# Kernel optimization log

Measured on AMD Instinct MI355X. Metric: run time of the kernel, lower is better.

Reference implementation:

```python
import jax, jax.numpy as jnp
import numpy as np

N_NODES = 100000
N_EDGES = 1600000
IN_DIM = 128
HID_DIM = 128
OUT_DIM = 16
N_GRAPHS = 128


def setup_inputs() -> dict:
    key = jax.random.key(0)
    ks = jax.random.split(key, 8)
    x = jax.random.normal(ks[0], (N_NODES, IN_DIM), dtype=jnp.float32)
    edge_index = jax.random.randint(ks[1], (2, N_EDGES), 0, N_NODES, dtype=jnp.int64)
    batch = jnp.sort(jax.random.randint(ks[2], (N_NODES,), 0, N_GRAPHS, dtype=jnp.int64))
    # GCNConv params (glorot-ish scale) and Linear params
    w1 = jax.random.normal(ks[3], (IN_DIM, HID_DIM), dtype=jnp.float32) / np.sqrt(IN_DIM)
    b1 = jnp.zeros((HID_DIM,), dtype=jnp.float32)
    w2 = jax.random.normal(ks[4], (HID_DIM, HID_DIM), dtype=jnp.float32) / np.sqrt(HID_DIM)
    b2 = jnp.zeros((HID_DIM,), dtype=jnp.float32)
    wc = jax.random.normal(ks[5], (HID_DIM, OUT_DIM), dtype=jnp.float32) / np.sqrt(HID_DIM)
    bc = jnp.zeros((OUT_DIM,), dtype=jnp.float32)
    return {"x": x, "edge_index": edge_index, "batch": batch,
            "w1": w1, "b1": b1, "w2": w2, "b2": b2, "wc": wc, "bc": bc}


def _gcn_layer(h, src, dst, w, b, n_nodes):
    # h: [N, Fin]; src/dst: [E+N] (self-loops already appended)
    h = h @ w  # [N, Fout]
    ones = jnp.ones_like(dst, dtype=h.dtype)
    deg = jax.ops.segment_sum(ones, dst, num_segments=n_nodes)  # [N]
    dinv = jnp.where(deg > 0, jax.lax.rsqrt(deg), 0.0)
    norm = dinv[src] * dinv[dst]  # [E+N]
    msg = h[src] * norm[:, None]  # gather + scale, [E+N, Fout]
    out = jax.ops.segment_sum(msg, dst, num_segments=n_nodes)  # scatter-add
    return out + b


def reference(x, edge_index, batch, w1, b1, w2, b2, wc, bc):
    n = x.shape[0]
    loop = jnp.arange(n, dtype=edge_index.dtype)
    src = jnp.concatenate([edge_index[0], loop])  # add self-loops (PyG default)
    dst = jnp.concatenate([edge_index[1], loop])

    h = jax.nn.relu(_gcn_layer(x, src, dst, w1, b1, n))
    h = jax.nn.relu(_gcn_layer(h, src, dst, w2, b2, n))

    # global mean pool over graphs
    sums = jax.ops.segment_sum(h, batch, num_segments=N_GRAPHS)  # [G, H]
    cnt = jax.ops.segment_sum(jnp.ones((n,), h.dtype), batch, num_segments=N_GRAPHS)
    pooled = sums / jnp.maximum(cnt, 1.0)[:, None]

    return pooled @ wc + bc  # [G, OUT_DIM]
```

## Files before the change

kernel.cpp:

```cpp
#include <hip/hip_runtime.h>
#include <stdint.h>

#define NN 100000
#define NE 1600000
#define FDIM 128
#define NGRAPH 128
#define ODIM 16
#define NBKT 391
#define CAP 4608
#define PCAP 8704
#define SCHUNK 2048
#define NSCAT ((NE + SCHUNK - 1) / SCHUNK)
#define NSTARTB ((NN + 255) / 256)

typedef __attribute__((ext_vector_type(8))) short short8;
typedef __attribute__((ext_vector_type(8))) unsigned short ushort8;
typedef __attribute__((ext_vector_type(4))) float f32x4;
typedef __attribute__((ext_vector_type(2))) float f32x2;

__device__ __forceinline__ float blo(unsigned int p) { return __uint_as_float(p << 16); }
__device__ __forceinline__ float bhi(unsigned int p) { return __uint_as_float(p & 0xffff0000u); }
__device__ __forceinline__ unsigned short f2b(float f) {
    unsigned int u = __float_as_uint(f);
    unsigned int r = (u + 0x7fffu + ((u >> 16) & 1u)) >> 16;
    return (unsigned short)r;
}
__device__ __forceinline__ unsigned int packbf(float lo, float hi) {
    return (unsigned int)f2b(lo) | ((unsigned int)f2b(hi) << 16);
}

__device__ __forceinline__ int detect_w(const int* __restrict__ ei) {
    int lane = threadIdx.x & 63;
    int v = ei[2 * lane + 1];
    return (__ballot(v != 0) == 0ULL) ? 1 : 0;
}
__device__ __forceinline__ int ld_idx(const int* __restrict__ p, long long i, int w) {
    return w ? p[2 * i] : p[i];
}

__global__ void __launch_bounds__(256) k_prep(
    const float* __restrict__ w1, const float* __restrict__ w2,
    unsigned short* __restrict__ wt1, unsigned short* __restrict__ wt2,
    const int* __restrict__ ei, const int* __restrict__ batch,
    int* __restrict__ gstart, int* __restrict__ bcursor,
    unsigned short* __restrict__ xws)
{
    int b = blockIdx.x, t = threadIdx.x;
    if (b < 128) {
        int idx = b * 256 + t;
        int which = idx >> 14, r = idx & 16383;
        int k = r >> 7, j = r & 127;
        const float* w = which ? w2 : w1;
        unsigned short* wt = which ? wt2 : wt1;
        wt[j * 128 + k] = f2b(w[k * 128 + j]);
    } else if (b < 128 + NSTARTB) {
        int w = detect_w(ei);
        int i = (b - 128) * 256 + t;
        if (i < NN) {
            int bb = ld_idx(batch, i, w);
            int prev = (i == 0) ? -1 : ld_idx(batch, i - 1, w);
            for (int g = prev + 1; g <= bb; ++g) gstart[g] = i;
            if (i == NN - 1)
                for (int g = bb + 1; g <= NGRAPH; ++g) gstart[g] = NN;
        }
    } else {
        int i = (b - 128 - NSTARTB) * 256 + t;
        if (i < NBKT) bcursor[i] = i * CAP;
        if (b == 128 + NSTARTB && t < FDIM) xws[(size_t)NN * FDIM + t] = 0;
    }
}

__global__ void __launch_bounds__(512) k_scat(const int* __restrict__ ei,
                                              int* __restrict__ bcursor,
                                              unsigned int* __restrict__ rec) {
    __shared__ int hist[NBKT];
    __shared__ int gbase[NBKT];
    __shared__ int lcur[NBKT];
    int t = threadIdx.x;
    int w = detect_w(ei);
    for (int i = t; i < NBKT; i += 512) hist[i] = 0;
    __syncthreads();
    long long e0 = (long long)blockIdx.x * SCHUNK;
    unsigned int myrec[4];
    int mybkt[4];
    #pragma unroll
    for (int j = 0; j < 4; ++j) {
        long long e = e0 + j * 512 + t;
        if (e < NE) {
            int s = ld_idx(ei, e, w);
            int d = ld_idx(ei, NE + e, w);
            mybkt[j] = d >> 8;
            myrec[j] = (unsigned int)s | ((unsigned int)(d & 255) << 17);
            atomicAdd(&hist[mybkt[j]], 1);
        } else mybkt[j] = -1;
    }
    __syncthreads();
    for (int i = t; i < NBKT; i += 512) {
        int c = hist[i];
        gbase[i] = c ? atomicAdd(&bcursor[i], c) : 0;
        lcur[i] = 0;
    }
    __syncthreads();
    #pragma unroll
    for (int j = 0; j < 4; ++j) {
        int b = mybkt[j];
        if (b >= 0) {
            int r = atomicAdd(&lcur[b], 1);
            int p = gbase[b] + r;
            if (p < (b + 1) * CAP) rec[p] = myrec[j];
        }
    }
}

__global__ void __launch_bounds__(256) k_bucket(const unsigned int* __restrict__ rec,
                                                const int* __restrict__ bcursor,
                                                int* __restrict__ csr,
                                                int* __restrict__ offs,
                                                int* __restrict__ deg,
                                                float* __restrict__ dinv) {
    __shared__ unsigned int rbuf[CAP];
    __shared__ int srcout[PCAP];
    __shared__ int hist[256], scn[256], cur[256];
    int b = blockIdx.x, t = threadIdx.x;
    int rbase = b * CAP;
    int cnt = bcursor[b] - rbase;
    if (cnt > CAP) cnt = CAP;
    hist[t] = 0;
    __syncthreads();
    for (int j = t; j < cnt; j += 256) {
        unsigned int r = rec[rbase + j];
        rbuf[j] = r;
        atomicAdd(&hist[r >> 17], 1);
    }
    for (int j = t; j < PCAP; j += 256) srcout[j] = NN << 8;
    __syncthreads();
    int node = (b << 8) + t;
    int v = hist[t];
    int pv = (node < NN) ? ((v + 16) & ~15) : 0;
    scn[t] = pv;
    __syncthreads();
    for (int o = 1; o < 256; o <<= 1) {
        int tv = (t >= o) ? scn[t - o] : 0;
        __syncthreads();
        scn[t] += tv;
        __syncthreads();
    }
    int pexcl = scn[t] - pv;
    cur[t] = pexcl;
    int obase = b * PCAP;
    if (node < NN) {
        offs[node] = obase + pexcl;
        deg[node] = pv;
        dinv[node] = rsqrtf((float)(v + 1));
        srcout[pexcl + v] = node << 8;
    }
    __syncthreads();
    for (int j = t; j < cnt; j += 256) {
        unsigned int r = rbuf[j];
        int p = atomicAdd(&cur[r >> 17], 1);
        srcout[p] = (int)(r & 0x1FFFFu) << 8;
    }
    __syncthreads();
    int total = scn[255];
    for (int j = t; j < total; j += 256) csr[obase + j] = srcout[j];
}

#define LWS 136
template <bool BF16IN>
__global__ void __launch_bounds__(256) k_gemm(
    const void* __restrict__ Xv,
    const unsigned short* __restrict__ WT,
    const float* __restrict__ dinv,
    unsigned short* __restrict__ OUT)
{
    __shared__ unsigned short lw[128 * LWS];
    int tid = threadIdx.x;
    for (int it = 0; it < 8; ++it) {
        int vidx = it * 256 + tid;
        int j = vidx >> 4, kc = vidx & 15;
        ushort8 v = *(const ushort8*)(WT + j * 128 + kc * 8);
        *(ushort8*)(&lw[j * LWS + kc * 8]) = v;
    }
    __syncthreads();

    int wave = tid >> 6, lane = tid & 63;
    int quad = lane >> 4, n16 = lane & 15;
    int row0 = (blockIdx.x * 4 + wave) * 16;
    if (row0 >= NN) return;

    f32x4 acc[8];
    for (int ct = 0; ct < 8; ++ct) acc[ct] = (f32x4){0.f, 0.f, 0.f, 0.f};

    const int arow = row0 + n16;
    for (int kk = 0; kk < 4; ++kk) {
        short8 a;
        if (BF16IN) {
            a = *(const short8*)((const unsigned short*)Xv + (size_t)arow * 128 + kk * 32 + quad * 8);
        } else {
            const float* ap = (const float*)Xv + (size_t)arow * 128 + kk * 32 + quad * 8;
            float4 a01 = *(const float4*)(ap);
            float4 a23 = *(const float4*)(ap + 4);
            a[0] = (short)f2b(a01.x); a[1] = (short)f2b(a01.y);
            a[2] = (short)f2b(a01.z); a[3] = (short)f2b(a01.w);
            a[4] = (short)f2b(a23.x); a[5] = (short)f2b(a23.y);
            a[6] = (short)f2b(a23.z); a[7] = (short)f2b(a23.w);
        }
        for (int ct = 0; ct < 8; ++ct) {
            short8 b = *(const short8*)(&lw[(ct * 16 + n16) * LWS + kk * 32 + quad * 8]);
            acc[ct] = __builtin_amdgcn_mfma_f32_16x16x32_bf16(a, b, acc[ct], 0, 0, 0);
        }
    }
    for (int r = 0; r < 4; ++r) {
        int row = row0 + quad * 4 + r;
        float dv = dinv[row];
        for (int ct = 0; ct < 8; ++ct)
            OUT[(size_t)row * 128 + ct * 16 + n16] = f2b(acc[ct][r] * dv);
    }
}

__device__ __forceinline__ void acc8(f32x2* a2, uint4 q) {
    a2[0] += (f32x2){blo(q.x), bhi(q.x)};
    a2[1] += (f32x2){blo(q.y), bhi(q.y)};
    a2[2] += (f32x2){blo(q.z), bhi(q.z)};
    a2[3] += (f32x2){blo(q.w), bhi(q.w)};
}

__global__ void __launch_bounds__(256) k_agg(
    const unsigned short* __restrict__ XWS,
    const int* __restrict__ csr,
    const int* __restrict__ offs,
    const int* __restrict__ deg,
    const float* __restrict__ dinv,
    const float* __restrict__ bias,
    unsigned short* __restrict__ H)
{
    int wave = threadIdx.x >> 6, lane = threadIdx.x & 63;
    int v = blockIdx.x * 4 + wave;
    int g = lane >> 4, f = lane & 15;
    int beg = offs[v], pdeg = deg[v];
    const char* xb = (const char*)XWS;
    unsigned fo = (unsigned)(f * 16);
    const int* cp = csr + beg + 4 * g;

    f32x2 a2[4];
    a2[0] = (f32x2){0.f, 0.f}; a2[1] = (f32x2){0.f, 0.f};
    a2[2] = (f32x2){0.f, 0.f}; a2[3] = (f32x2){0.f, 0.f};

    for (int j = 0; j < pdeg; j += 16) {
        int4 c = *(const int4*)(cp + j);
        uint4 q0 = *(const uint4*)(xb + ((unsigned)c.x + fo));
        uint4 q1 = *(const uint4*)(xb + ((unsigned)c.y + fo));
        uint4 q2 = *(const uint4*)(xb + ((unsigned)c.z + fo));
        uint4 q3 = *(const uint4*)(xb + ((unsigned)c.w + fo));
        acc8(a2, q0);
        acc8(a2, q1);
        acc8(a2, q2);
        acc8(a2, q3);
    }
    #pragma unroll
    for (int i = 0; i < 4; ++i) {
        a2[i].x += __shfl_xor(a2[i].x, 16);
        a2[i].y += __shfl_xor(a2[i].y, 16);
        a2[i].x += __shfl_xor(a2[i].x, 32);
        a2[i].y += __shfl_xor(a2[i].y, 32);
    }
    if (g == 0) {
        float dv = dinv[v];
        float4 b0 = *(const float4*)(bias + f * 8);
        float4 b1 = *(const float4*)(bias + f * 8 + 4);
        uint4 o;
        o.x = packbf(fmaxf(fmaf(a2[0].x, dv, b0.x), 0.f), fmaxf(fmaf(a2[0].y, dv, b0.y), 0.f));
        o.y = packbf(fmaxf(fmaf(a2[1].x, dv, b0.z), 0.f), fmaxf(fmaf(a2[1].y, dv, b0.w), 0.f));
        o.z = packbf(fmaxf(fmaf(a2[2].x, dv, b1.x), 0.f), fmaxf(fmaf(a2[2].y, dv, b1.y), 0.f));
        o.w = packbf(fmaxf(fmaf(a2[3].x, dv, b1.z), 0.f), fmaxf(fmaf(a2[3].y, dv, b1.w), 0.f));
        *(uint4*)(H + (size_t)v * FDIM + f * 8) = o;
    }
}

__global__ void __launch_bounds__(256) k_poolcls(
    const unsigned short* __restrict__ H, const int* __restrict__ gstart,
    const float* __restrict__ wc, const float* __restrict__ bc,
    float* __restrict__ out)
{
    __shared__ float red[512];
    __shared__ float pl[FDIM];
    int g = blockIdx.x;
    int t = threadIdx.x;
    int pair = t & 63;
    int seg = t >> 6;
    int beg = gstart[g], end = gstart[g + 1];
    float a0 = 0.f, a1 = 0.f;
    for (int i = beg + seg; i < end; i += 4) {
        unsigned int q = *(const unsigned int*)(H + (size_t)i * FDIM + 2 * pair);
        a0 += blo(q); a1 += bhi(q);
    }
    red[t] = a0; red[256 + t] = a1;
    __syncthreads();
    if (seg == 0) {
        a0 = red[t] + red[t + 64] + red[t + 128] + red[t + 192];
        a1 = red[256 + t] + red[256 + t + 64] + red[256 + t + 128] + red[256 + t + 192];
        float inv = 1.f / fmaxf((float)(end - beg), 1.f);
        pl[2 * pair] = a0 * inv;
        pl[2 * pair + 1] = a1 * inv;
    }
    __syncthreads();
    int o = t & 15, fs = t >> 4;
    float acc = 0.f;
    #pragma unroll
    for (int k = 0; k < 8; ++k)
        acc += pl[fs * 8 + k] * wc[(fs * 8 + k) * ODIM + o];
    red[t] = acc;
    __syncthreads();
    if (t < 16) {
        float s = bc[t];
        #pragma unroll
        for (int k = 0; k < 16; ++k) s += red[k * 16 + t];
        out[g * ODIM + t] = s;
    }
}

extern "C" void kernel_launch(void* const* d_in, const int* in_sizes, int n_in,
                              void* d_out, int out_size, void* d_ws, size_t ws_size,
                              hipStream_t stream) {
    const float* x   = (const float*)d_in[0];
    const int* ei    = (const int*)d_in[1];
    const int* batch = (const int*)d_in[2];
    const float* w1  = (const float*)d_in[3];
    const float* b1  = (const float*)d_in[4];
    const float* w2  = (const float*)d_in[5];
    const float* b2  = (const float*)d_in[6];
    const float* wc  = (const float*)d_in[7];
    const float* bc  = (const float*)d_in[8];
    float* out = (float*)d_out;

    char* ws = (char*)d_ws;
    size_t off = 0;
    auto alloc = [&](size_t bytes) -> void* {
        off = (off + 255) & ~(size_t)255;
        void* p = ws + off;
        off += bytes;
        return p;
    };
    int*   bcursor = (int*)alloc(NBKT * 4);
    int*   offs    = (int*)alloc(NN * 4);
    int*   deg     = (int*)alloc(NN * 4);
    float* dinv    = (float*)alloc(NN * 4);
    int*   gstart  = (int*)alloc((NGRAPH + 1) * 4);
    unsigned int* rec = (unsigned int*)alloc((size_t)NBKT * CAP * 4);
    int*   csr     = (int*)alloc((size_t)NBKT * PCAP * 4 + 256);
    unsigned short* wt1 = (unsigned short*)alloc(128 * 128 * 2);
    unsigned short* wt2 = (unsigned short*)alloc(128 * 128 * 2);
    unsigned short* xws = (unsigned short*)alloc((size_t)(NN + 1) * FDIM * 2);
    unsigned short* h   = (unsigned short*)alloc((size_t)NN * FDIM * 2);

    k_prep<<<128 + NSTARTB + 2, 256, 0, stream>>>(w1, w2, wt1, wt2, ei, batch, gstart, bcursor, xws);
    k_scat<<<NSCAT, 512, 0, stream>>>(ei, bcursor, rec);
    k_bucket<<<NBKT, 256, 0, stream>>>(rec, bcursor, csr, offs, deg, dinv);

    k_gemm<false><<<(NN / 16 + 3) / 4, 256, 0, stream>>>(x, wt1, dinv, xws);
    k_agg<<<NN / 4, 256, 0, stream>>>(xws, csr, offs, deg, dinv, b1, h);
    k_gemm<true><<<(NN / 16 + 3) / 4, 256, 0, stream>>>(h, wt2, dinv, xws);
    k_agg<<<NN / 4, 256, 0, stream>>>(xws, csr, offs, deg, dinv, b2, h);
    k_poolcls<<<NGRAPH, 256, 0, stream>>>(h, gstart, wc, bc, out);
}
```

Before: 342.3 us.

## Unroll aggregation gathers, pack offsets/degree, widen scatter and pool blocks

The aggregation loop is unrolled to issue eight row gathers per iteration, and the CSR index reads use nontemporal loads. Offsets and padded degree are packed into one int2 so each node needs a single load. The scatter kernel handles twice as many edges per block, and the pooling kernel runs 512 threads. Manual bf16 rounding is replaced with the HIP packed float2-to-bf16 conversion. The changes aim to raise memory-level parallelism and cut instruction count, at the cost of extra register pressure and fewer scatter blocks.

```diff
diff --git a/kernel.cpp b/kernel.cpp
--- a/kernel.cpp
+++ b/kernel.cpp
@@ -1,4 +1,5 @@
 #include <hip/hip_runtime.h>
+#include <hip/hip_bf16.h>
 #include <stdint.h>
 
 #define NN 100000
@@ -9,7 +10,7 @@
 #define NBKT 391
 #define CAP 4608
 #define PCAP 8704
-#define SCHUNK 2048
+#define SCHUNK 4096
 #define NSCAT ((NE + SCHUNK - 1) / SCHUNK)
 #define NSTARTB ((NN + 255) / 256)
 
@@ -17,6 +18,7 @@
 typedef __attribute__((ext_vector_type(8))) unsigned short ushort8;
 typedef __attribute__((ext_vector_type(4))) float f32x4;
 typedef __attribute__((ext_vector_type(2))) float f32x2;
+typedef __attribute__((ext_vector_type(4))) int i32x4;
 
 __device__ __forceinline__ float blo(unsigned int p) { return __uint_as_float(p << 16); }
 __device__ __forceinline__ float bhi(unsigned int p) { return __uint_as_float(p & 0xffff0000u); }
@@ -25,8 +27,9 @@
     unsigned int r = (u + 0x7fffu + ((u >> 16) & 1u)) >> 16;
     return (unsigned short)r;
 }
-__device__ __forceinline__ unsigned int packbf(float lo, float hi) {
-    return (unsigned int)f2b(lo) | ((unsigned int)f2b(hi) << 16);
+__device__ __forceinline__ unsigned int cvt2(float lo, float hi) {
+    __hip_bfloat162 b = __float22bfloat162_rn(float2{lo, hi});
+    return *reinterpret_cast<unsigned int*>(&b);
 }
 
 __device__ __forceinline__ int detect_w(const int* __restrict__ ei) {
@@ -81,10 +84,10 @@
     for (int i = t; i < NBKT; i += 512) hist[i] = 0;
     __syncthreads();
     long long e0 = (long long)blockIdx.x * SCHUNK;
-    unsigned int myrec[4];
-    int mybkt[4];
+    unsigned int myrec[8];
+    int mybkt[8];
     #pragma unroll
-    for (int j = 0; j < 4; ++j) {
+    for (int j = 0; j < 8; ++j) {
         long long e = e0 + j * 512 + t;
         if (e < NE) {
             int s = ld_idx(ei, e, w);
@@ -102,7 +105,7 @@
     }
     __syncthreads();
     #pragma unroll
-    for (int j = 0; j < 4; ++j) {
+    for (int j = 0; j < 8; ++j) {
         int b = mybkt[j];
         if (b >= 0) {
             int r = atomicAdd(&lcur[b], 1);
@@ -115,8 +118,7 @@
 __global__ void __launch_bounds__(256) k_bucket(const unsigned int* __restrict__ rec,
                                                 const int* __restrict__ bcursor,
                                                 int* __restrict__ csr,
-                                                int* __restrict__ offs,
-                                                int* __restrict__ deg,
+                                                int2* __restrict__ odeg,
                                                 float* __restrict__ dinv) {
     __shared__ unsigned int rbuf[CAP];
     __shared__ int srcout[PCAP];
@@ -128,7 +130,7 @@
     hist[t] = 0;
     __syncthreads();
     for (int j = t; j < cnt; j += 256) {
-        unsigned int r = rec[rbase + j];
+        unsigned int r = __builtin_nontemporal_load(&rec[rbase + j]);
         rbuf[j] = r;
         atomicAdd(&hist[r >> 17], 1);
     }
@@ -149,8 +151,7 @@
     cur[t] = pexcl;
     int obase = b * PCAP;
     if (node < NN) {
-        offs[node] = obase + pexcl;
-        deg[node] = pv;
+        odeg[node] = make_int2(obase + pexcl, pv);
         dinv[node] = rsqrtf((float)(v + 1));
         srcout[pexcl + v] = node << 8;
     }
@@ -200,10 +201,12 @@
             const float* ap = (const float*)Xv + (size_t)arow * 128 + kk * 32 + quad * 8;
             float4 a01 = *(const float4*)(ap);
             float4 a23 = *(const float4*)(ap + 4);
-            a[0] = (short)f2b(a01.x); a[1] = (short)f2b(a01.y);
-            a[2] = (short)f2b(a01.z); a[3] = (short)f2b(a01.w);
-            a[4] = (short)f2b(a23.x); a[5] = (short)f2b(a23.y);
-            a[6] = (short)f2b(a23.z); a[7] = (short)f2b(a23.w);
+            uint4 P;
+            P.x = cvt2(a01.x, a01.y);
+            P.y = cvt2(a01.z, a01.w);
+            P.z = cvt2(a23.x, a23.y);
+            P.w = cvt2(a23.z, a23.w);
+            a = *(short8*)&P;
         }
         for (int ct = 0; ct < 8; ++ct) {
             short8 b = *(const short8*)(&lw[(ct * 16 + n16) * LWS + kk * 32 + quad * 8]);
@@ -228,8 +231,7 @@
 __global__ void __launch_bounds__(256) k_agg(
     const unsigned short* __restrict__ XWS,
     const int* __restrict__ csr,
-    const int* __restrict__ offs,
-    const int* __restrict__ deg,
+    const int2* __restrict__ odeg,
     const float* __restrict__ dinv,
     const float* __restrict__ bias,
     unsigned short* __restrict__ H)
@@ -237,7 +239,8 @@
     int wave = threadIdx.x >> 6, lane = threadIdx.x & 63;
     int v = blockIdx.x * 4 + wave;
     int g = lane >> 4, f = lane & 15;
-    int beg = offs[v], pdeg = deg[v];
+    int2 od = odeg[v];
+    int beg = od.x, pdeg = od.y;
     const char* xb = (const char*)XWS;
     unsigned fo = (unsigned)(f * 16);
     const int* cp = csr + beg + 4 * g;
@@ -246,16 +249,29 @@
     a2[0] = (f32x2){0.f, 0.f}; a2[1] = (f32x2){0.f, 0.f};
     a2[2] = (f32x2){0.f, 0.f}; a2[3] = (f32x2){0.f, 0.f};
 
-    for (int j = 0; j < pdeg; j += 16) {
-        int4 c = *(const int4*)(cp + j);
-        uint4 q0 = *(const uint4*)(xb + ((unsigned)c.x + fo));
-        uint4 q1 = *(const uint4*)(xb + ((unsigned)c.y + fo));
-        uint4 q2 = *(const uint4*)(xb + ((unsigned)c.z + fo));
-        uint4 q3 = *(const uint4*)(xb + ((unsigned)c.w + fo));
-        acc8(a2, q0);
-        acc8(a2, q1);
-        acc8(a2, q2);
-        acc8(a2, q3);
+    int j = 0;
+    int pd2 = pdeg & ~31;
+    for (; j < pd2; j += 32) {
+        i32x4 ca = __builtin_nontemporal_load((const i32x4*)(cp + j));
+        i32x4 cb = __builtin_nontemporal_load((const i32x4*)(cp + j + 16));
+        uint4 q0 = *(const uint4*)(xb + ((unsigned)ca.x + fo));
+        uint4 q1 = *(const uint4*)(xb + ((unsigned)ca.y + fo));
+        uint4 q2 = *(const uint4*)(xb + ((unsigned)ca.z + fo));
+        uint4 q3 = *(const uint4*)(xb + ((unsigned)ca.w + fo));
+        uint4 q4 = *(const uint4*)(xb + ((unsigned)cb.x + fo));
+        uint4 q5 = *(const uint4*)(xb + ((unsigned)cb.y + fo));
+        uint4 q6 = *(const uint4*)(xb + ((unsigned)cb.z + fo));
+        uint4 q7 = *(const uint4*)(xb + ((unsigned)cb.w + fo));
+        acc8(a2, q0); acc8(a2, q1); acc8(a2, q2); acc8(a2, q3);
+        acc8(a2, q4); acc8(a2, q5); acc8(a2, q6); acc8(a2, q7);
+    }
+    if (j < pdeg) {
+        i32x4 ca = __builtin_nontemporal_load((const i32x4*)(cp + j));
+        uint4 q0 = *(const uint4*)(xb + ((unsigned)ca.x + fo));
+        uint4 q1 = *(const uint4*)(xb + ((unsigned)ca.y + fo));
+        uint4 q2 = *(const uint4*)(xb + ((unsigned)ca.z + fo));
+        uint4 q3 = *(const uint4*)(xb + ((unsigned)ca.w + fo));
+        acc8(a2, q0); acc8(a2, q1); acc8(a2, q2); acc8(a2, q3);
     }
     #pragma unroll
     for (int i = 0; i < 4; ++i) {
@@ -269,20 +285,20 @@
         float4 b0 = *(const float4*)(bias + f * 8);
         float4 b1 = *(const float4*)(bias + f * 8 + 4);
         uint4 o;
-        o.x = packbf(fmaxf(fmaf(a2[0].x, dv, b0.x), 0.f), fmaxf(fmaf(a2[0].y, dv, b0.y), 0.f));
-        o.y = packbf(fmaxf(fmaf(a2[1].x, dv, b0.z), 0.f), fmaxf(fmaf(a2[1].y, dv, b0.w), 0.f));
-        o.z = packbf(fmaxf(fmaf(a2[2].x, dv, b1.x), 0.f), fmaxf(fmaf(a2[2].y, dv, b1.y), 0.f));
-        o.w = packbf(fmaxf(fmaf(a2[3].x, dv, b1.z), 0.f), fmaxf(fmaf(a2[3].y, dv, b1.w), 0.f));
+        o.x = cvt2(fmaxf(fmaf(a2[0].x, dv, b0.x), 0.f), fmaxf(fmaf(a2[0].y, dv, b0.y), 0.f));
+        o.y = cvt2(fmaxf(fmaf(a2[1].x, dv, b0.z), 0.f), fmaxf(fmaf(a2[1].y, dv, b0.w), 0.f));
+        o.z = cvt2(fmaxf(fmaf(a2[2].x, dv, b1.x), 0.f), fmaxf(fmaf(a2[2].y, dv, b1.y), 0.f));
+        o.w = cvt2(fmaxf(fmaf(a2[3].x, dv, b1.z), 0.f), fmaxf(fmaf(a2[3].y, dv, b1.w), 0.f));
         *(uint4*)(H + (size_t)v * FDIM + f * 8) = o;
     }
 }
 
-__global__ void __launch_bounds__(256) k_poolcls(
+__global__ void __launch_bounds__(512) k_poolcls(
     const unsigned short* __restrict__ H, const int* __restrict__ gstart,
     const float* __restrict__ wc, const float* __restrict__ bc,
     float* __restrict__ out)
 {
-    __shared__ float red[512];
+    __shared__ float red[1024];
     __shared__ float pl[FDIM];
     int g = blockIdx.x;
     int t = threadIdx.x;
@@ -290,26 +306,32 @@
     int seg = t >> 6;
     int beg = gstart[g], end = gstart[g + 1];
     float a0 = 0.f, a1 = 0.f;
-    for (int i = beg + seg; i < end; i += 4) {
+    for (int i = beg + seg; i < end; i += 8) {
         unsigned int q = *(const unsigned int*)(H + (size_t)i * FDIM + 2 * pair);
         a0 += blo(q); a1 += bhi(q);
     }
-    red[t] = a0; red[256 + t] = a1;
+    red[t] = a0; red[512 + t] = a1;
     __syncthreads();
     if (seg == 0) {
-        a0 = red[t] + red[t + 64] + red[t + 128] + red[t + 192];
-        a1 = red[256 + t] + red[256 + t + 64] + red[256 + t + 128] + red[256 + t + 192];
+        float s0 = 0.f, s1 = 0.f;
+        #pragma unroll
+        for (int k = 0; k < 8; ++k) {
+            s0 += red[pair + 64 * k];
+            s1 += red[512 + pair + 64 * k];
+        }
         float inv = 1.f / fmaxf((float)(end - beg), 1.f);
-        pl[2 * pair] = a0 * inv;
-        pl[2 * pair + 1] = a1 * inv;
-    }
-    __syncthreads();
-    int o = t & 15, fs = t >> 4;
-    float acc = 0.f;
-    #pragma unroll
-    for (int k = 0; k < 8; ++k)
-        acc += pl[fs * 8 + k] * wc[(fs * 8 + k) * ODIM + o];
-    red[t] = acc;
+        pl[2 * pair] = s0 * inv;
+        pl[2 * pair + 1] = s1 * inv;
+    }
+    __syncthreads();
+    if (t < 256) {
+        int o = t & 15, fs = t >> 4;
+        float acc = 0.f;
+        #pragma unroll
+        for (int k = 0; k < 8; ++k)
+            acc += pl[fs * 8 + k] * wc[(fs * 8 + k) * ODIM + o];
+        red[t] = acc;
+    }
     __syncthreads();
     if (t < 16) {
         float s = bc[t];
@@ -342,8 +364,7 @@
         return p;
     };
     int*   bcursor = (int*)alloc(NBKT * 4);
-    int*   offs    = (int*)alloc(NN * 4);
-    int*   deg     = (int*)alloc(NN * 4);
+    int2*  odeg    = (int2*)alloc((size_t)NN * 8);
     float* dinv    = (float*)alloc(NN * 4);
     int*   gstart  = (int*)alloc((NGRAPH + 1) * 4);
     unsigned int* rec = (unsigned int*)alloc((size_t)NBKT * CAP * 4);
@@ -355,11 +376,11 @@
 
     k_prep<<<128 + NSTARTB + 2, 256, 0, stream>>>(w1, w2, wt1, wt2, ei, batch, gstart, bcursor, xws);
     k_scat<<<NSCAT, 512, 0, stream>>>(ei, bcursor, rec);
-    k_bucket<<<NBKT, 256, 0, stream>>>(rec, bcursor, csr, offs, deg, dinv);
+    k_bucket<<<NBKT, 256, 0, stream>>>(rec, bcursor, csr, odeg, dinv);
 
     k_gemm<false><<<(NN / 16 + 3) / 4, 256, 0, stream>>>(x, wt1, dinv, xws);
-    k_agg<<<NN / 4, 256, 0, stream>>>(xws, csr, offs, deg, dinv, b1, h);
+    k_agg<<<NN / 4, 256, 0, stream>>>(xws, csr, odeg, dinv, b1, h);
     k_gemm<true><<<(NN / 16 + 3) / 4, 256, 0, stream>>>(h, wt2, dinv, xws);
-    k_agg<<<NN / 4, 256, 0, stream>>>(xws, csr, offs, deg, dinv, b2, h);
-    k_poolcls<<<NGRAPH, 256, 0, stream>>>(h, gstart, wc, bc, out);
-}
+    k_agg<<<NN / 4, 256, 0, stream>>>(xws, csr, odeg, dinv, b2, h);
+    k_poolcls<<<NGRAPH, 512, 0, stream>>>(h, gstart, wc, bc, out);
+}
```

Result: faster. 312.8 us (-8.6%).
